# Kernel tuning notes

Measured on AMD Instinct MI355X. Metric: run time of the kernel, lower is better.

## Reference

```python
import jax, jax.numpy as jnp
import numpy as np

N_NODES, N_EDGES, N_CH, D = 50000, 400000, 4, 128
N_SUB, SUB_SZ = 2048, 64

def setup_inputs() -> dict:
    key = jax.random.key(0)
    ks = jax.random.split(key, 5)
    x = jax.random.normal(ks[0], (N_NODES, N_CH, D), dtype=jnp.float32)
    edge_index = jax.random.randint(ks[1], (2, N_EDGES), 0, N_NODES)
    edge_weight = jax.random.uniform(ks[2], (N_EDGES,), dtype=jnp.float32)
    subG_node = jax.random.randint(ks[3], (N_SUB, SUB_SZ), 0, N_NODES)
    W = jax.random.normal(ks[4], (D, D), dtype=jnp.float32) / jnp.sqrt(jnp.float32(D))
    return {"x": x, "edge_index": edge_index, "edge_weight": edge_weight,
            "subG_node": subG_node, "W": W}

def reference(x, edge_index, edge_weight, subG_node, W):
    n = x.shape[0]
    src, dst = edge_index[0], edge_index[1]
    # per-channel conv loop vectorized: same conv weight applied to every channel
    h = jnp.einsum('ncd,de->nce', x, W)            # [N, C, D]
    msg = h[src] * edge_weight[:, None, None]       # [E, C, D] weighted messages
    agg = jax.ops.segment_sum(msg, dst, num_segments=n)  # [N, C, D]
    emb = agg.mean(axis=1)                          # channel mean -> [N, D]
    # pos2sp + spmm == masked gather + sum over subgraph members
    mask = subG_node >= 0                           # -1 entries are padding
    idx = jnp.where(mask, subG_node, 0)
    pooled = jnp.sum(emb[idx] * mask[..., None].astype(emb.dtype), axis=1)  # [n_sub, D]
    return pooled
```

## Files before the change

kernel.cpp:

```cpp
#include <hip/hip_runtime.h>

#define N_NODES 50000
#define N_EDGES 400000
#define N_CH    4
#define DIM     128
#define N_SUB   2048
#define SUB_SZ  64
#define CAP     64


__device__ __forceinline__ unsigned f2bf(float f) {
    unsigned u = __float_as_uint(f);
    return (u + 0x7FFFu + ((u >> 16) & 1u)) >> 16;
}
__device__ __forceinline__ float bf2f(unsigned h) {
    return __uint_as_float(h << 16);
}

__global__ __launch_bounds__(256) void cm_kernel(const float* __restrict__ x,
                                                 uint2* __restrict__ ybf,
                                                 int* __restrict__ cnt) {
    int i = blockIdx.x * blockDim.x + threadIdx.x;
    if (i < N_NODES) cnt[i] = 0;
    if (i >= N_NODES * 32) return;
    int n  = i >> 5;
    int d4 = i & 31;
    const float4* xb = (const float4*)(x + (size_t)n * N_CH * DIM) + d4;
    float4 a = xb[0 * 32];
    float4 b = xb[1 * 32];
    float4 c = xb[2 * 32];
    float4 d = xb[3 * 32];
    float r0 = 0.25f * (a.x + b.x + c.x + d.x);
    float r1 = 0.25f * (a.y + b.y + c.y + d.y);
    float r2 = 0.25f * (a.z + b.z + c.z + d.z);
    float r3 = 0.25f * (a.w + b.w + c.w + d.w);
    uint2 p;
    p.x = f2bf(r0) | (f2bf(r1) << 16);
    p.y = f2bf(r2) | (f2bf(r3) << 16);
    ybf[(size_t)n * 32 + d4] = p;
}

__global__ __launch_bounds__(256) void fill_kernel(const int* __restrict__ ei,
                                                   const float* __restrict__ ew,
                                                   int* __restrict__ cnt,
                                                   int2* __restrict__ csr) {
    int e = blockIdx.x * blockDim.x + threadIdx.x;
    if (e >= N_EDGES) return;
    int src = ei[e];
    int dst = ei[N_EDGES + e];
    int slot = atomicAdd(&cnt[dst], 1);
    if (slot < CAP)
        csr[(size_t)dst * CAP + slot] = make_int2(src, __float_as_int(ew[e]));
}

__global__ __launch_bounds__(256) void gather_kernel(const int* __restrict__ cnt,
                                                     const int2* __restrict__ csr,
                                                     const uint2* __restrict__ ybf,
                                                     uint2* __restrict__ zbf) {
    int t  = blockIdx.x * blockDim.x + threadIdx.x;
    int n  = t >> 5;
    int d4 = t & 31;
    if (n >= N_NODES) return;
    int deg = cnt[n];
    if (deg > CAP) deg = CAP;
    const int2* row = csr + (size_t)n * CAP;
    float4 acc = make_float4(0.f, 0.f, 0.f, 0.f);
    for (int base = 0; base < deg; base += 32) {
        int k = base + d4;
        int2 e = make_int2(0, 0);
        if (k < deg) e = row[k];
        int c = deg - base;
        if (c > 32) c = 32;
        for (int j = 0; j < c; ++j) {
            int   srcn = __shfl(e.x, j, 32);
            float w    = __int_as_float(__shfl(e.y, j, 32));
            uint2 p = ybf[(size_t)srcn * 32 + d4];
            acc.x += w * bf2f(p.x & 0xFFFFu);
            acc.y += w * bf2f(p.x >> 16);
            acc.z += w * bf2f(p.y & 0xFFFFu);
            acc.w += w * bf2f(p.y >> 16);
        }
    }
    uint2 o;
    o.x = f2bf(acc.x) | (f2bf(acc.y) << 16);
    o.y = f2bf(acc.z) | (f2bf(acc.w) << 16);
    zbf[(size_t)n * 32 + d4] = o;
}

__global__ __launch_bounds__(128) void pool_gemm_kernel(const int* __restrict__ sub,
                                                        const unsigned short* __restrict__ zbf,
                                                        const float* __restrict__ Wm,
                                                        float* __restrict__ out) {
    __shared__ float emb[DIM];
    __shared__ int   idx[SUB_SZ];
    int s = blockIdx.x;
    int t = threadIdx.x;
    if (t < SUB_SZ) idx[t] = sub[s * SUB_SZ + t];
    __syncthreads();
    float acc = 0.f;
    for (int j = 0; j < SUB_SZ; ++j) {
        int n = idx[j];
        if (n >= 0) acc += bf2f(zbf[(size_t)n * DIM + t]);
    }
    emb[t] = acc;
    __syncthreads();
    float o = 0.f;
#pragma unroll 8
    for (int d = 0; d < DIM; ++d) {
        o += emb[d] * Wm[d * DIM + t];
    }
    out[s * DIM + t] = o;
}

extern "C" void kernel_launch(void* const* d_in, const int* in_sizes, int n_in,
                              void* d_out, int out_size, void* d_ws, size_t ws_size,
                              hipStream_t stream) {
    const float* x   = (const float*)d_in[0];
    const int*   ei  = (const int*)  d_in[1];
    const float* ew  = (const float*)d_in[2];
    const int*   sub = (const int*)  d_in[3];
    const float* Wm  = (const float*)d_in[4];
    float*       out = (float*)d_out;

    char* ws = (char*)d_ws;
    uint2* ybf = (uint2*)ws;   ws += (size_t)N_NODES * DIM * 2;
    uint2* zbf = (uint2*)ws;   ws += (size_t)N_NODES * DIM * 2;
    int*   cnt = (int*)ws;     ws += (size_t)N_NODES * 4;
    int2*  csr = (int2*)ws;

    cm_kernel<<<(N_NODES * 32 + 255) / 256, 256, 0, stream>>>(x, ybf, cnt);

    fill_kernel<<<(N_EDGES + 255) / 256, 256, 0, stream>>>(ei, ew, cnt, csr);

    gather_kernel<<<(N_NODES * 32 + 255) / 256, 256, 0, stream>>>(cnt, csr, ybf, zbf);

    pool_gemm_kernel<<<N_SUB, 128, 0, stream>>>(sub, (const unsigned short*)zbf, Wm, out);
}
```

Baseline: 237.2 us.

## Fuse all stages into one cooperative persistent kernel with grid syncs

Replaces four separate kernel launches with one cooperative kernel of 1024 blocks that runs the count reset, CSR fill, channel mean, neighbor gather, and pooling+GEMM stages. The stages are separated by grid-wide barriers and use grid-stride loops. The pool stage now handles two subgraphs per 256-thread block. The intent is to remove launch gaps between kernels, at the cost of grid.sync overhead and less occupancy flexibility than independent launches.

```diff
diff --git a/kernel.cpp b/kernel.cpp
--- a/kernel.cpp
+++ b/kernel.cpp
@@ -1,4 +1,7 @@
 #include <hip/hip_runtime.h>
+#include <hip/hip_cooperative_groups.h>
+
+namespace cg = cooperative_groups;
 
 #define N_NODES 50000
 #define N_EDGES 400000
@@ -7,6 +10,9 @@
 #define N_SUB   2048
 #define SUB_SZ  64
 #define CAP     64
+
+#define GRID_BLKS 1024
+#define BLK       256
 
 
 __device__ __forceinline__ unsigned f2bf(float f) {
@@ -17,99 +23,106 @@
     return __uint_as_float(h << 16);
 }
 
-__global__ __launch_bounds__(256) void cm_kernel(const float* __restrict__ x,
-                                                 uint2* __restrict__ ybf,
-                                                 int* __restrict__ cnt) {
-    int i = blockIdx.x * blockDim.x + threadIdx.x;
-    if (i < N_NODES) cnt[i] = 0;
-    if (i >= N_NODES * 32) return;
-    int n  = i >> 5;
-    int d4 = i & 31;
-    const float4* xb = (const float4*)(x + (size_t)n * N_CH * DIM) + d4;
-    float4 a = xb[0 * 32];
-    float4 b = xb[1 * 32];
-    float4 c = xb[2 * 32];
-    float4 d = xb[3 * 32];
-    float r0 = 0.25f * (a.x + b.x + c.x + d.x);
-    float r1 = 0.25f * (a.y + b.y + c.y + d.y);
-    float r2 = 0.25f * (a.z + b.z + c.z + d.z);
-    float r3 = 0.25f * (a.w + b.w + c.w + d.w);
-    uint2 p;
-    p.x = f2bf(r0) | (f2bf(r1) << 16);
-    p.y = f2bf(r2) | (f2bf(r3) << 16);
-    ybf[(size_t)n * 32 + d4] = p;
-}
+__global__ __launch_bounds__(BLK, 4)
+void fused_kernel(const float* __restrict__ x,
+                  const int* __restrict__ ei,
+                  const float* __restrict__ ew,
+                  const int* __restrict__ sub,
+                  const float* __restrict__ Wm,
+                  float* __restrict__ out,
+                  uint2* __restrict__ ybf,
+                  unsigned short* __restrict__ zbf,
+                  int* __restrict__ cnt,
+                  int2* __restrict__ csr) {
+    cg::grid_group grid = cg::this_grid();
+    const int gsz = GRID_BLKS * BLK;
+    const int tid = blockIdx.x * BLK + threadIdx.x;
 
-__global__ __launch_bounds__(256) void fill_kernel(const int* __restrict__ ei,
-                                                   const float* __restrict__ ew,
-                                                   int* __restrict__ cnt,
-                                                   int2* __restrict__ csr) {
-    int e = blockIdx.x * blockDim.x + threadIdx.x;
-    if (e >= N_EDGES) return;
-    int src = ei[e];
-    int dst = ei[N_EDGES + e];
-    int slot = atomicAdd(&cnt[dst], 1);
-    if (slot < CAP)
-        csr[(size_t)dst * CAP + slot] = make_int2(src, __float_as_int(ew[e]));
-}
+    for (int i = tid; i < N_NODES; i += gsz) cnt[i] = 0;
+    __threadfence();
+    grid.sync();
 
-__global__ __launch_bounds__(256) void gather_kernel(const int* __restrict__ cnt,
-                                                     const int2* __restrict__ csr,
-                                                     const uint2* __restrict__ ybf,
-                                                     uint2* __restrict__ zbf) {
-    int t  = blockIdx.x * blockDim.x + threadIdx.x;
-    int n  = t >> 5;
-    int d4 = t & 31;
-    if (n >= N_NODES) return;
-    int deg = cnt[n];
-    if (deg > CAP) deg = CAP;
-    const int2* row = csr + (size_t)n * CAP;
-    float4 acc = make_float4(0.f, 0.f, 0.f, 0.f);
-    for (int base = 0; base < deg; base += 32) {
-        int k = base + d4;
-        int2 e = make_int2(0, 0);
-        if (k < deg) e = row[k];
-        int c = deg - base;
-        if (c > 32) c = 32;
-        for (int j = 0; j < c; ++j) {
-            int   srcn = __shfl(e.x, j, 32);
-            float w    = __int_as_float(__shfl(e.y, j, 32));
-            uint2 p = ybf[(size_t)srcn * 32 + d4];
-            acc.x += w * bf2f(p.x & 0xFFFFu);
-            acc.y += w * bf2f(p.x >> 16);
-            acc.z += w * bf2f(p.y & 0xFFFFu);
-            acc.w += w * bf2f(p.y >> 16);
+    for (int e = tid; e < N_EDGES; e += gsz) {
+        int src = ei[e];
+        int dst = ei[N_EDGES + e];
+        int slot = atomicAdd(&cnt[dst], 1);
+        if (slot < CAP)
+            csr[(size_t)dst * CAP + slot] = make_int2(src, __float_as_int(ew[e]));
+    }
+    for (int i = tid; i < N_NODES * 32; i += gsz) {
+        int n  = i >> 5;
+        int d4 = i & 31;
+        const float4* xb = (const float4*)(x + (size_t)n * N_CH * DIM) + d4;
+        float4 a = xb[0 * 32];
+        float4 b = xb[1 * 32];
+        float4 c = xb[2 * 32];
+        float4 d = xb[3 * 32];
+        float r0 = 0.25f * (a.x + b.x + c.x + d.x);
+        float r1 = 0.25f * (a.y + b.y + c.y + d.y);
+        float r2 = 0.25f * (a.z + b.z + c.z + d.z);
+        float r3 = 0.25f * (a.w + b.w + c.w + d.w);
+        uint2 p;
+        p.x = f2bf(r0) | (f2bf(r1) << 16);
+        p.y = f2bf(r2) | (f2bf(r3) << 16);
+        ybf[(size_t)n * 32 + d4] = p;
+    }
+    __threadfence();
+    grid.sync();
+
+    for (int i = tid; i < N_NODES * 32; i += gsz) {
+        int n  = i >> 5;
+        int d4 = i & 31;
+        int deg = cnt[n];
+        if (deg > CAP) deg = CAP;
+        const int2* row = csr + (size_t)n * CAP;
+        float4 acc = make_float4(0.f, 0.f, 0.f, 0.f);
+        for (int base = 0; base < deg; base += 32) {
+            int k = base + d4;
+            int2 e = make_int2(0, 0);
+            if (k < deg) e = row[k];
+            int c = deg - base;
+            if (c > 32) c = 32;
+            for (int j = 0; j < c; ++j) {
+                int   srcn = __shfl(e.x, j, 32);
+                float w    = __int_as_float(__shfl(e.y, j, 32));
+                uint2 p = ybf[(size_t)srcn * 32 + d4];
+                acc.x += w * bf2f(p.x & 0xFFFFu);
+                acc.y += w * bf2f(p.x >> 16);
+                acc.z += w * bf2f(p.y & 0xFFFFu);
+                acc.w += w * bf2f(p.y >> 16);
+            }
         }
+        uint2 o;
+        o.x = f2bf(acc.x) | (f2bf(acc.y) << 16);
+        o.y = f2bf(acc.z) | (f2bf(acc.w) << 16);
+        ((uint2*)zbf)[(size_t)n * 32 + d4] = o;
     }
-    uint2 o;
-    o.x = f2bf(acc.x) | (f2bf(acc.y) << 16);
-    o.y = f2bf(acc.z) | (f2bf(acc.w) << 16);
-    zbf[(size_t)n * 32 + d4] = o;
-}
+    __threadfence();
+    grid.sync();
 
-__global__ __launch_bounds__(128) void pool_gemm_kernel(const int* __restrict__ sub,
-                                                        const unsigned short* __restrict__ zbf,
-                                                        const float* __restrict__ Wm,
-                                                        float* __restrict__ out) {
-    __shared__ float emb[DIM];
-    __shared__ int   idx[SUB_SZ];
-    int s = blockIdx.x;
-    int t = threadIdx.x;
-    if (t < SUB_SZ) idx[t] = sub[s * SUB_SZ + t];
-    __syncthreads();
-    float acc = 0.f;
-    for (int j = 0; j < SUB_SZ; ++j) {
-        int n = idx[j];
-        if (n >= 0) acc += bf2f(zbf[(size_t)n * DIM + t]);
+    __shared__ float emb[2][DIM];
+    __shared__ int   idx[2][SUB_SZ];
+    for (int sb = blockIdx.x; sb < N_SUB / 2; sb += GRID_BLKS) {
+        int half = threadIdx.x >> 7;
+        int t    = threadIdx.x & 127;
+        int s    = sb * 2 + half;
+        if (t < SUB_SZ) idx[half][t] = sub[s * SUB_SZ + t];
+        __syncthreads();
+        float acc = 0.f;
+        for (int j = 0; j < SUB_SZ; ++j) {
+            int n = idx[half][j];
+            if (n >= 0) acc += bf2f(zbf[(size_t)n * DIM + t]);
+        }
+        emb[half][t] = acc;
+        __syncthreads();
+        float o = 0.f;
+#pragma unroll 8
+        for (int d = 0; d < DIM; ++d) {
+            o += emb[half][d] * Wm[d * DIM + t];
+        }
+        out[s * DIM + t] = o;
+        __syncthreads();
     }
-    emb[t] = acc;
-    __syncthreads();
-    float o = 0.f;
-#pragma unroll 8
-    for (int d = 0; d < DIM; ++d) {
-        o += emb[d] * Wm[d * DIM + t];
-    }
-    out[s * DIM + t] = o;
 }
 
 extern "C" void kernel_launch(void* const* d_in, const int* in_sizes, int n_in,
@@ -123,16 +136,13 @@
     float*       out = (float*)d_out;
 
     char* ws = (char*)d_ws;
-    uint2* ybf = (uint2*)ws;   ws += (size_t)N_NODES * DIM * 2;
-    uint2* zbf = (uint2*)ws;   ws += (size_t)N_NODES * DIM * 2;
-    int*   cnt = (int*)ws;     ws += (size_t)N_NODES * 4;
-    int2*  csr = (int2*)ws;
+    uint2*          ybf = (uint2*)ws;          ws += (size_t)N_NODES * DIM * 2;
+    unsigned short* zbf = (unsigned short*)ws; ws += (size_t)N_NODES * DIM * 2;
+    int*            cnt = (int*)ws;            ws += (size_t)N_NODES * 4;
+    int2*           csr = (int2*)ws;
 
-    cm_kernel<<<(N_NODES * 32 + 255) / 256, 256, 0, stream>>>(x, ybf, cnt);
-
-    fill_kernel<<<(N_EDGES + 255) / 256, 256, 0, stream>>>(ei, ew, cnt, csr);
-
-    gather_kernel<<<(N_NODES * 32 + 255) / 256, 256, 0, stream>>>(cnt, csr, ybf, zbf);
-
-    pool_gemm_kernel<<<N_SUB, 128, 0, stream>>>(sub, (const unsigned short*)zbf, Wm, out);
+    void* args[] = { (void*)&x, (void*)&ei, (void*)&ew, (void*)&sub, (void*)&Wm,
+                     (void*)&out, (void*)&ybf, (void*)&zbf, (void*)&cnt, (void*)&csr };
+    hipLaunchCooperativeKernel((const void*)fused_kernel,
+                               dim3(GRID_BLKS), dim3(BLK), args, 0, stream);
 }
```

Result: slower. 823.7 us (+247.2%).
